# Kernel optimization log

Measured on AMD Instinct MI355X. Metric: run time of the kernel, lower is better.

Reference implementation:

```python
import jax, jax.numpy as jnp
import numpy as np

BLOCK_GRID = 128   # blocks per side at full res (each 8x8 full-res pixels)
BLOCK_FR = 8       # full-res block side
C = 128
NUMBER_POOL = 3


def _build_mask():
    # block values cycle 0..3 -> exactly 4096 blocks per level; mask is (1,1,1024,1024)
    bv = (np.add.outer(np.arange(BLOCK_GRID), np.arange(BLOCK_GRID)) % 4).astype(np.int32)
    return np.kron(bv, np.ones((BLOCK_FR, BLOCK_FR), np.int32))[None, None]


def setup_inputs() -> dict:
    key = jax.random.key(0)
    mask = _build_mask()
    npool = NUMBER_POOL
    start_idx = sum(int((mask == i).sum()) // (2 ** i) for i in range(npool - 1))
    s = 2 ** (npool - 1)
    n_cur = int((mask[:, :, ::s, ::s] >= npool - 1).sum())
    N = start_idx + n_cur  # 425984
    x = jax.random.normal(key, (1, C, N), dtype=jnp.float32)
    return {"input": x, "pooling_mask": jnp.asarray(mask), "number_pool": npool}


def reference(input, pooling_mask, number_pool):
    # mask logic is data-dependent-shape -> resolve indices with concrete numpy
    mask = np.asarray(pooling_mask)
    start_idx = 0
    for i in range(number_pool - 1):
        start_idx += int((mask == i).sum()) // (2 ** i)
    g_hi = input[:, :, :start_idx]          # passthrough higher-res tokens
    g_cur = input[:, :, start_idx:]          # current-res tokens
    s = 2 ** (number_pool - 1)
    mask_cr = mask[:, :, ::s, ::s]           # (1,1,H,W) current-res level map
    H, W = mask_cr.shape[2], mask_cr.shape[3]
    Cc = input.shape[1]
    cur_flat = (mask_cr >= number_pool - 1).reshape(-1)
    idx_cur = np.nonzero(cur_flat)[0]        # scatter targets for g_cur
    dont = (mask_cr == number_pool - 1).reshape(-1)[idx_cur]
    out_dont = g_cur[:, :, np.nonzero(dont)[0]]
    touch = (mask_cr >= number_pool)[:, :, ::2, ::2].reshape(-1)
    idx_touch = np.nonzero(touch)[0]         # gather sources from pooled grid
    # scatter ragged tokens into dense -inf buffer
    buf = jnp.full((1, Cc, H * W), -np.inf, dtype=input.dtype)
    buf = buf.at[:, :, idx_cur].set(g_cur).reshape(1, Cc, H, W)
    # 2x2/stride-2 max pool
    pooled = jax.lax.reduce_window(buf, -np.inf, jax.lax.max,
                                   (1, 1, 2, 2), (1, 1, 2, 2), 'VALID')
    out_lo = pooled.reshape(1, Cc, -1)[:, :, idx_touch]
    return jnp.concatenate([g_hi, out_dont, out_lo], axis=2)
```

## Files before the change

kernel.cpp:

```cpp
#include <hip/hip_runtime.h>


namespace {
constexpr int kC     = 128;
constexpr int kNIn   = 425984;
constexpr int kNOut  = 413696;
constexpr int kStart = 393216;
constexpr int kNDont = 16384;

__global__ void copy_hi(const float* __restrict__ in, float* __restrict__ out) {
    const int c  = blockIdx.y;
    const int n4 = blockIdx.x * blockDim.x + threadIdx.x;
    const float4 v = *reinterpret_cast<const float4*>(in + (size_t)c * kNIn + (size_t)n4 * 4);
    *reinterpret_cast<float4*>(out + (size_t)c * kNOut + (size_t)n4 * 4) = v;
}

__global__ void tail(const float* __restrict__ in, float* __restrict__ out) {
    const int c = blockIdx.y;
    const int t = blockIdx.x * blockDim.x + threadIdx.x;
    const int u = t >> 5;
    const int g = t & 31;

    const float* gc = in + (size_t)c * kNIn + kStart + 256 * u + 4 * g;
    const float4 r0 = *reinterpret_cast<const float4*>(gc);
    const float4 r1 = *reinterpret_cast<const float4*>(gc + 128);

    float* ob = out + (size_t)c * kNOut + kStart;
    float2 d0, d1;
    float lo;
    if ((u & 3) == 3) {
        d0 = make_float2(r0.z, r0.w);
        d1 = make_float2(r1.z, r1.w);
        lo = fmaxf(fmaxf(r0.x, r0.y), fmaxf(r1.x, r1.y));
    } else {
        d0 = make_float2(r0.x, r0.y);
        d1 = make_float2(r1.x, r1.y);
        lo = fmaxf(fmaxf(r0.z, r0.w), fmaxf(r1.z, r1.w));
    }
    *reinterpret_cast<float2*>(ob + 128 * u + 2 * g)      = d0;
    *reinterpret_cast<float2*>(ob + 128 * u + 64 + 2 * g) = d1;
    ob[kNDont + 32 * u + g] = lo;
}
}

extern "C" void kernel_launch(void* const* d_in, const int* in_sizes, int n_in,
                              void* d_out, int out_size, void* d_ws, size_t ws_size,
                              hipStream_t stream) {
    const float* in = (const float*)d_in[0];
    float* out = (float*)d_out;
    copy_hi<<<dim3(kStart / 4 / 256, kC), 256, 0, stream>>>(in, out);
    tail<<<dim3(4096 / 256, kC), 256, 0, stream>>>(in, out);
}
```

Before: 80.95 us.

## Fuse passthrough copy and pooling tail into one grid-stride kernel

Merges the bulk passthrough copy and the pooled tail into a single launch where each thread copies 24 float4 chunks in an unrolled loop and then handles its tail element. All stores become nontemporal. This removes one kernel launch and the many tiny copy blocks, at the cost of a much smaller grid (2048 blocks), which may limit memory-level parallelism for a ~420 MB bandwidth-bound copy.

```diff
diff --git a/kernel.cpp b/kernel.cpp
--- a/kernel.cpp
+++ b/kernel.cpp
@@ -2,44 +2,52 @@
 
 
 namespace {
+typedef float f32x4 __attribute__((ext_vector_type(4)));
+typedef float f32x2 __attribute__((ext_vector_type(2)));
+
 constexpr int kC     = 128;
 constexpr int kNIn   = 425984;
 constexpr int kNOut  = 413696;
 constexpr int kStart = 393216;
 constexpr int kNDont = 16384;
+constexpr int kTPC   = 4096;
+constexpr int kIters = kStart / 4 / kTPC;
 
-__global__ void copy_hi(const float* __restrict__ in, float* __restrict__ out) {
-    const int c  = blockIdx.y;
-    const int n4 = blockIdx.x * blockDim.x + threadIdx.x;
-    const float4 v = *reinterpret_cast<const float4*>(in + (size_t)c * kNIn + (size_t)n4 * 4);
-    *reinterpret_cast<float4*>(out + (size_t)c * kNOut + (size_t)n4 * 4) = v;
-}
-
-__global__ void tail(const float* __restrict__ in, float* __restrict__ out) {
+__global__ __launch_bounds__(256) void fused(const float* __restrict__ in,
+                                             float* __restrict__ out) {
     const int c = blockIdx.y;
     const int t = blockIdx.x * blockDim.x + threadIdx.x;
+    const float* inc = in + (size_t)c * kNIn;
+    float* outc = out + (size_t)c * kNOut;
+
     const int u = t >> 5;
     const int g = t & 31;
+    const float* gc = inc + kStart + 256 * u + 4 * g;
+    const f32x4 r0 = *reinterpret_cast<const f32x4*>(gc);
+    const f32x4 r1 = *reinterpret_cast<const f32x4*>(gc + 128);
 
-    const float* gc = in + (size_t)c * kNIn + kStart + 256 * u + 4 * g;
-    const float4 r0 = *reinterpret_cast<const float4*>(gc);
-    const float4 r1 = *reinterpret_cast<const float4*>(gc + 128);
+#pragma unroll 8
+    for (int k = 0; k < kIters; ++k) {
+        const int n4 = t + k * kTPC;
+        const f32x4 v = *reinterpret_cast<const f32x4*>(inc + (size_t)n4 * 4);
+        __builtin_nontemporal_store(v, reinterpret_cast<f32x4*>(outc + (size_t)n4 * 4));
+    }
 
-    float* ob = out + (size_t)c * kNOut + kStart;
-    float2 d0, d1;
+    f32x2 d0, d1;
     float lo;
     if ((u & 3) == 3) {
-        d0 = make_float2(r0.z, r0.w);
-        d1 = make_float2(r1.z, r1.w);
+        d0 = f32x2{r0.z, r0.w};
+        d1 = f32x2{r1.z, r1.w};
         lo = fmaxf(fmaxf(r0.x, r0.y), fmaxf(r1.x, r1.y));
     } else {
-        d0 = make_float2(r0.x, r0.y);
-        d1 = make_float2(r1.x, r1.y);
+        d0 = f32x2{r0.x, r0.y};
+        d1 = f32x2{r1.x, r1.y};
         lo = fmaxf(fmaxf(r0.z, r0.w), fmaxf(r1.z, r1.w));
     }
-    *reinterpret_cast<float2*>(ob + 128 * u + 2 * g)      = d0;
-    *reinterpret_cast<float2*>(ob + 128 * u + 64 + 2 * g) = d1;
-    ob[kNDont + 32 * u + g] = lo;
+    float* ob = outc + kStart;
+    __builtin_nontemporal_store(d0, reinterpret_cast<f32x2*>(ob + 128 * u + 2 * g));
+    __builtin_nontemporal_store(d1, reinterpret_cast<f32x2*>(ob + 128 * u + 64 + 2 * g));
+    __builtin_nontemporal_store(lo, ob + kNDont + 32 * u + g);
 }
 }
 
@@ -48,6 +56,5 @@
                               hipStream_t stream) {
     const float* in = (const float*)d_in[0];
     float* out = (float*)d_out;
-    copy_hi<<<dim3(kStart / 4 / 256, kC), 256, 0, stream>>>(in, out);
-    tail<<<dim3(4096 / 256, kC), 256, 0, stream>>>(in, out);
+    fused<<<dim3(kTPC / 256, kC), 256, 0, stream>>>(in, out);
 }
```

New measurement: 66.99 us. 17.3% less time.
